# Kernel optimization log

Hardware: AMD Instinct MI355X
Metric: run time of the kernel (lower is better)

Reference implementation:

```python
import jax, jax.numpy as jnp
import numpy as np

E = 8       # num experts
T = 1024    # num tokens
H = 1024    # hidden dim
I = 1024    # intermediate dim (per gate/up half)


def setup_inputs() -> dict:
    key = jax.random.key(0)
    k1, k2, k3, k4 = jax.random.split(key, 4)
    return {
        "hidden_states": jax.random.normal(k1, (T, H), jnp.float32),
        "router_logits": jax.random.normal(k2, (T, E), jnp.float32),
        # W13 stored pre-transposed as in the module: [E, H, 2*I]
        "W13": jax.random.normal(k3, (E, H, 2 * I), jnp.float32) * 0.02,
        # W2 stored pre-transposed: [E, I, H]
        "W2": jax.random.normal(k4, (E, I, H), jnp.float32) * 0.02,
        "top_k": 2,
    }


def reference(hidden_states, router_logits, W13, W2, top_k):
    num_experts = router_logits.shape[-1]
    # --- routing: topk_softmax (softmax over all experts, then top-k) ---
    probs = jax.nn.softmax(router_logits, axis=-1)            # [T, E]
    w, idx = jax.lax.top_k(probs, top_k)                      # [T, K]
    # renormalize=True path of moe_gather
    w = w / jnp.sum(w, axis=-1, keepdims=True)
    # combine weights per expert: [T, E]
    combine = jnp.sum(jax.nn.one_hot(idx, num_experts, dtype=w.dtype) * w[..., None], axis=1)
    # --- grouped gate-up GEMM + silu_and_mul ---
    h13 = jnp.einsum('th,ehf->tef', hidden_states, W13)       # [T, E, 2I]
    gate, up = jnp.split(h13, 2, axis=-1)                     # each [T, E, I]
    act = jax.nn.silu(gate) * up                              # silu_and_mul
    # --- grouped down GEMM ---
    down = jnp.einsum('tei,eih->teh', act, W2)                # [T, E, H]
    # --- combine (moe_gather) ---
    return jnp.einsum('te,teh->th', combine, down)            # [T, H]
```

## Files before the change

### kernel.cpp

```cpp
#include <hip/hip_runtime.h>
#include <hip/hip_bf16.h>
#include <stdint.h>

#define NE    8
#define NTOK  1024
#define NH    1024
#define NI    1024
#define NPAIR 2048

typedef __attribute__((ext_vector_type(8))) short short8;
typedef __attribute__((ext_vector_type(4))) float f32x4;
typedef unsigned short u16;
typedef unsigned int   u32;

__device__ __forceinline__ u16 f2bf(float x) {
    union { float f; u32 u; } v; v.f = x;
    return (u16)((v.u + 0x7fffu + ((v.u >> 16) & 1u)) >> 16);
}

__device__ __forceinline__ void async_ld16(u16* lds, const u16* g) {
    __builtin_amdgcn_global_load_lds(
        (const __attribute__((address_space(1))) u32*)g,
        (__attribute__((address_space(3))) u32*)lds, 16, 0, 0);
}

__global__ __launch_bounds__(256) void route_kernel(
    const float* __restrict__ logits,
    int* __restrict__ counts, int* __restrict__ pair_tok,
    int2* __restrict__ t2p, float2* __restrict__ t2w)
{
    __shared__ int s_cnt[NE];
    __shared__ int s_base[NE];
    const int tid = threadIdx.x;
    if (tid < NE) s_cnt[tid] = 0;
    __syncthreads();

    int eA[4][2]; int slotA[4][2]; float wA[4][2];

    #pragma unroll
    for (int i = 0; i < 4; i++) {
        const int t = tid * 4 + i;
        float l[NE];
        #pragma unroll
        for (int e = 0; e < NE; e++) l[e] = logits[t * NE + e];
        int i0 = 0;
        #pragma unroll
        for (int e = 1; e < NE; e++) if (l[e] > l[i0]) i0 = e;
        int i1 = -1;
        #pragma unroll
        for (int e = 0; e < NE; e++) {
            if (e == i0) continue;
            if (i1 < 0 || l[e] > l[i1]) i1 = e;
        }
        const float e10 = __expf(l[i1] - l[i0]);
        const float inv = 1.0f / (1.0f + e10);
        eA[i][0] = i0; eA[i][1] = i1;
        wA[i][0] = inv; wA[i][1] = e10 * inv;
        slotA[i][0] = atomicAdd(&s_cnt[i0], 1);
        slotA[i][1] = atomicAdd(&s_cnt[i1], 1);
    }
    __syncthreads();
    if (tid == 0) {
        int acc = 0;
        #pragma unroll
        for (int e = 0; e < NE; e++) { s_base[e] = acc; acc += s_cnt[e]; }
    }
    __syncthreads();
    if (tid < NE) counts[tid] = s_cnt[tid];
    #pragma unroll
    for (int i = 0; i < 4; i++) {
        const int t = tid * 4 + i;
        const int p0 = s_base[eA[i][0]] + slotA[i][0];
        const int p1 = s_base[eA[i][1]] + slotA[i][1];
        pair_tok[p0] = t;
        pair_tok[p1] = t;
        t2p[t] = make_int2(p0, p1);
        t2w[t] = make_float2(wA[i][0], wA[i][1]);
    }
}

__device__ __forceinline__ bool find_tile(
    const int* __restrict__ counts, int tile, int bm, int ntn,
    int& e_o, int& mt_o, int& nt_o, int& cnt_o, int& base_o)
{
    int base = 0;
    #pragma unroll
    for (int e = 0; e < NE; e++) {
        const int cnt = counts[e];
        const int mtiles = (cnt + bm - 1) / bm;
        const int tiles = mtiles * ntn;
        if (tile < tiles) {
            e_o = e; mt_o = tile / ntn; nt_o = tile - (tile / ntn) * ntn;
            cnt_o = cnt; base_o = base; return true;
        }
        tile -= tiles; base += cnt;
    }
    return false;
}

__global__ __launch_bounds__(256) void cvt_x_kernel(
    const float* __restrict__ src, u16* __restrict__ dst)
{
    const int i = blockIdx.x * 256 + threadIdx.x;
    const float4* s = (const float4*)src;
    const float4 a = s[2 * i], b = s[2 * i + 1];
    uint4 o;
    o.x = f2bf(a.x) | ((u32)f2bf(a.y) << 16);
    o.y = f2bf(a.z) | ((u32)f2bf(a.w) << 16);
    o.z = f2bf(b.x) | ((u32)f2bf(b.y) << 16);
    o.w = f2bf(b.z) | ((u32)f2bf(b.w) << 16);
    *(uint4*)(dst + (size_t)i * 8) = o;
}

__global__ __launch_bounds__(256) void cvt_tr_kernel(
    const float* __restrict__ src, u16* __restrict__ dst, int K, int N)
{
    __shared__ float Ts[64][65];
    const int ktiles = K >> 6, ntiles = N >> 6;
    const int tpe = ktiles * ntiles;
    const int e = blockIdx.x / tpe;
    const int rem = blockIdx.x - e * tpe;
    const int kt = rem / ntiles, nt = rem - (rem / ntiles) * ntiles;
    const float* sb = src + ((size_t)e * K + (size_t)kt * 64) * N + nt * 64;
    const int tid = threadIdx.x;

    #pragma unroll
    for (int i = 0; i < 4; i++) {
        const int idx = tid + i * 256;
        const int r = idx >> 4, c = (idx & 15) << 2;
        const float4 v = *(const float4*)(sb + (size_t)r * N + c);
        Ts[r][c + 0] = v.x; Ts[r][c + 1] = v.y;
        Ts[r][c + 2] = v.z; Ts[r][c + 3] = v.w;
    }
    __syncthreads();
    u16* db = dst + ((size_t)e * N + (size_t)nt * 64) * K + kt * 64;
    #pragma unroll
    for (int i = 0; i < 2; i++) {
        const int u = tid + i * 256;
        const int n = u >> 3, k8 = (u & 7) << 3;
        uint4 o;
        o.x = f2bf(Ts[k8 + 0][n]) | ((u32)f2bf(Ts[k8 + 1][n]) << 16);
        o.y = f2bf(Ts[k8 + 2][n]) | ((u32)f2bf(Ts[k8 + 3][n]) << 16);
        o.z = f2bf(Ts[k8 + 4][n]) | ((u32)f2bf(Ts[k8 + 5][n]) << 16);
        o.w = f2bf(Ts[k8 + 6][n]) | ((u32)f2bf(Ts[k8 + 7][n]) << 16);
        *(uint4*)(db + (size_t)n * K + k8) = o;
    }
}

__global__ __launch_bounds__(256) void gemm1_kernel(
    const u16* __restrict__ Xb, const u16* __restrict__ W13t,
    const int* __restrict__ counts, const int* __restrict__ pair_tok,
    u16* __restrict__ act)
{
    int e, mt, nt, cnt, base;
    if (!find_tile(counts, blockIdx.x, 128, NI / 64, e, mt, nt, cnt, base)) return;

    __shared__ u16 As[128 * 32];
    __shared__ u16 Bs[128 * 32];

    const int tid = threadIdx.x;
    const int ct = nt * 64;

    const int ra = tid >> 2, sa = (tid & 3) << 3;
    const int t0 = pair_tok[base + min(mt * 128 + ra, cnt - 1)];
    const int t1 = pair_tok[base + min(mt * 128 + 64 + ra, cnt - 1)];
    const u16* ga0 = Xb + (size_t)t0 * NH + sa;
    const u16* ga1 = Xb + (size_t)t1 * NH + sa;
    u16* la0 = As + tid * 8;
    u16* la1 = As + (tid + 256) * 8;

    const u16* gb0 = W13t + ((size_t)e * 2048 + ct + ra) * 1024 + sa;
    const u16* gb1 = W13t + ((size_t)e * 2048 + 1024 + ct + ra) * 1024 + sa;
    u16* lb0 = Bs + tid * 8;
    u16* lb1 = Bs + (tid + 256) * 8;

    const int lane = tid & 63, w = tid >> 6;
    const int quad = lane >> 4, lid = lane & 15;
    const int rw = w >> 1, cw = w & 1;

    const short8* afp[4];
    const short8* bgp[2];
    const short8* bup[2];
    #pragma unroll
    for (int mi = 0; mi < 4; mi++)
        afp[mi] = (const short8*)(As + (rw * 64 + mi * 16 + lid) * 32 + quad * 8);
    #pragma unroll
    for (int nj = 0; nj < 2; nj++) {
        bgp[nj] = (const short8*)(Bs + (cw * 32 + nj * 16 + lid) * 32 + quad * 8);
        bup[nj] = (const short8*)(Bs + (64 + cw * 32 + nj * 16 + lid) * 32 + quad * 8);
    }

    f32x4 accg[4][2] = {};
    f32x4 accu[4][2] = {};

    for (int k0 = 0; k0 < NH; k0 += 32) {
        async_ld16(la0, ga0 + k0);
        async_ld16(la1, ga1 + k0);
        async_ld16(lb0, gb0 + k0);
        async_ld16(lb1, gb1 + k0);
        __syncthreads();
        short8 a[4], bg[2], bu[2];
        #pragma unroll
        for (int mi = 0; mi < 4; mi++) a[mi] = *afp[mi];
        #pragma unroll
        for (int nj = 0; nj < 2; nj++) { bg[nj] = *bgp[nj]; bu[nj] = *bup[nj]; }
        #pragma unroll
        for (int mi = 0; mi < 4; mi++) {
            #pragma unroll
            for (int nj = 0; nj < 2; nj++) {
                accg[mi][nj] = __builtin_amdgcn_mfma_f32_16x16x32_bf16(a[mi], bg[nj], accg[mi][nj], 0, 0, 0);
                accu[mi][nj] = __builtin_amdgcn_mfma_f32_16x16x32_bf16(a[mi], bu[nj], accu[mi][nj], 0, 0, 0);
            }
        }
        __syncthreads();
    }

    #pragma unroll
    for (int mi = 0; mi < 4; mi++) {
        #pragma unroll
        for (int nj = 0; nj < 2; nj++) {
            const int col = ct + cw * 32 + nj * 16 + lid;
            #pragma unroll
            for (int r = 0; r < 4; r++) {
                const int row = mt * 128 + rw * 64 + mi * 16 + quad * 4 + r;
                if (row < cnt) {
                    const float g = accg[mi][nj][r], u = accu[mi][nj][r];
                    const float s = g / (1.0f + __expf(-g)) * u;
                    act[(size_t)(base + row) * NI + col] = f2bf(s);
                }
            }
        }
    }
}

__global__ __launch_bounds__(256) void gemm2_kernel(
    const u16* __restrict__ act, const u16* __restrict__ W2t,
    const int* __restrict__ counts, float* __restrict__ down)
{
    int e, mt, nt, cnt, base;
    if (!find_tile(counts, blockIdx.x, 64, NH / 128, e, mt, nt, cnt, base)) return;

    __shared__ u16 As[64 * 32];
    __shared__ u16 Bs[128 * 32];

    const int tid = threadIdx.x;
    const int ct = nt * 128;

    const int ra = tid >> 2, sa = (tid & 3) << 3;
    const int prow = base + min(mt * 64 + ra, cnt - 1);
    const u16* ga = act + (size_t)prow * NI + sa;
    u16* la = As + tid * 8;

    const u16* gb0 = W2t + ((size_t)e * 1024 + ct + ra) * NI + sa;
    const u16* gb1 = W2t + ((size_t)e * 1024 + ct + 64 + ra) * NI + sa;
    u16* lb0 = Bs + tid * 8;
    u16* lb1 = Bs + (tid + 256) * 8;

    const int lane = tid & 63, w = tid >> 6;
    const int quad = lane >> 4, lid = lane & 15;

    const short8* afp[4];
    const short8* bfp[2];
    #pragma unroll
    for (int mi = 0; mi < 4; mi++)
        afp[mi] = (const short8*)(As + (mi * 16 + lid) * 32 + quad * 8);
    #pragma unroll
    for (int nj = 0; nj < 2; nj++)
        bfp[nj] = (const short8*)(Bs + (w * 32 + nj * 16 + lid) * 32 + quad * 8);

    f32x4 acc[4][2] = {};

    for (int k0 = 0; k0 < NI; k0 += 32) {
        async_ld16(la, ga + k0);
        async_ld16(lb0, gb0 + k0);
        async_ld16(lb1, gb1 + k0);
        __syncthreads();
        short8 a[4], b[2];
        #pragma unroll
        for (int mi = 0; mi < 4; mi++) a[mi] = *afp[mi];
        #pragma unroll
        for (int nj = 0; nj < 2; nj++) b[nj] = *bfp[nj];
        #pragma unroll
        for (int mi = 0; mi < 4; mi++) {
            #pragma unroll
            for (int nj = 0; nj < 2; nj++)
                acc[mi][nj] = __builtin_amdgcn_mfma_f32_16x16x32_bf16(a[mi], b[nj], acc[mi][nj], 0, 0, 0);
        }
        __syncthreads();
    }

    #pragma unroll
    for (int mi = 0; mi < 4; mi++) {
        #pragma unroll
        for (int nj = 0; nj < 2; nj++) {
            const int col = ct + w * 32 + nj * 16 + lid;
            #pragma unroll
            for (int r = 0; r < 4; r++) {
                const int row = mt * 64 + mi * 16 + quad * 4 + r;
                if (row < cnt)
                    down[(size_t)(base + row) * NH + col] = acc[mi][nj][r];
            }
        }
    }
}

__global__ __launch_bounds__(256) void combine_kernel(
    const float* __restrict__ down, const int2* __restrict__ t2p,
    const float2* __restrict__ t2w, float* __restrict__ out)
{
    const int i = blockIdx.x * 256 + threadIdx.x;
    const int t = i >> 8;
    const int c = (i & 255) << 2;
    const int2 p = t2p[t];
    const float2 wv = t2w[t];
    const float4 d0 = *(const float4*)(down + (size_t)p.x * NH + c);
    const float4 d1 = *(const float4*)(down + (size_t)p.y * NH + c);
    float4 o;
    o.x = wv.x * d0.x + wv.y * d1.x;
    o.y = wv.x * d0.y + wv.y * d1.y;
    o.z = wv.x * d0.z + wv.y * d1.z;
    o.w = wv.x * d0.w + wv.y * d1.w;
    *(float4*)(out + (size_t)t * NH + c) = o;
}

extern "C" void kernel_launch(void* const* d_in, const int* in_sizes, int n_in,
                              void* d_out, int out_size, void* d_ws, size_t ws_size,
                              hipStream_t stream)
{
    const float* X      = (const float*)d_in[0];
    const float* logits = (const float*)d_in[1];
    const float* W13    = (const float*)d_in[2];
    const float* W2     = (const float*)d_in[3];
    float* out = (float*)d_out;

    char* ws = (char*)d_ws;
    int*    counts   = (int*)(ws + 0);
    int*    pair_tok = (int*)(ws + 256);
    int2*   t2p      = (int2*)(ws + 256 + 8192);
    float2* t2w      = (float2*)(ws + 256 + 16384);
    u16*    Xb       = (u16*)(ws + 65536);
    u16*    W13t     = (u16*)(ws + 4194304);
    u16*    W2t      = (u16*)(ws + 4194304 + 33554432);
    u16*    act      = (u16*)(ws + 54525952);
    float*  down     = (float*)(ws + 58720256);

    route_kernel<<<1, 256, 0, stream>>>(logits, counts, pair_tok, t2p, t2w);
    cvt_x_kernel<<<512, 256, 0, stream>>>(X, Xb);
    cvt_tr_kernel<<<NE * 16 * 32, 256, 0, stream>>>(W13, W13t, NH, 2 * NI);
    cvt_tr_kernel<<<NE * 16 * 16, 256, 0, stream>>>(W2, W2t, NI, NH);

    const int grid1 = (NPAIR / 128 + NE - 1) * (NI / 64);
    const int grid2 = (NPAIR / 64 + NE - 1) * (NH / 128);
    gemm1_kernel<<<grid1, 256, 0, stream>>>(Xb, W13t, counts, pair_tok, act);
    gemm2_kernel<<<grid2, 256, 0, stream>>>(act, W2t, counts, down);
    combine_kernel<<<NTOK * NH / 1024, 256, 0, stream>>>(down, t2p, t2w, out);
}
```

Before: 196.0 us.

## Fuse weight bf16 conversion into GEMMs and combine into gemm2 via atomics

Removes the separate transpose-and-convert kernels for W13 and W2. The GEMMs now read fp32 weights directly, convert them to bf16 in registers and store them into padded LDS, with a register prefetch of the next k-slice. This drops the extra full pass over the weights and the workspace writes. The combine kernel is also removed: gemm2 scales its results by the routing weight and atomically adds them into a zeroed output, which avoids the down buffer round trip but adds atomics and a memset. The fp32 weight loads are strided column reads, 4 bytes per lane, which may coalesce worse than the previous 16-byte async loads, and each weight is reloaded once per m-tile.

After: 205.1 us. 4.6% more time.

```diff
diff --git a/kernel.cpp b/kernel.cpp
--- a/kernel.cpp
+++ b/kernel.cpp
@@ -6,7 +6,9 @@
 #define NTOK  1024
 #define NH    1024
 #define NI    1024
+#define N13   2048
 #define NPAIR 2048
+#define SROW  40
 
 typedef __attribute__((ext_vector_type(8))) short short8;
 typedef __attribute__((ext_vector_type(4))) float f32x4;
@@ -18,16 +20,19 @@
     return (u16)((v.u + 0x7fffu + ((v.u >> 16) & 1u)) >> 16);
 }
 
-__device__ __forceinline__ void async_ld16(u16* lds, const u16* g) {
-    __builtin_amdgcn_global_load_lds(
-        (const __attribute__((address_space(1))) u32*)g,
-        (__attribute__((address_space(3))) u32*)lds, 16, 0, 0);
+__device__ __forceinline__ uint4 pack8(const float* f) {
+    uint4 o;
+    o.x = f2bf(f[0]) | ((u32)f2bf(f[1]) << 16);
+    o.y = f2bf(f[2]) | ((u32)f2bf(f[3]) << 16);
+    o.z = f2bf(f[4]) | ((u32)f2bf(f[5]) << 16);
+    o.w = f2bf(f[6]) | ((u32)f2bf(f[7]) << 16);
+    return o;
 }
 
 __global__ __launch_bounds__(256) void route_kernel(
     const float* __restrict__ logits,
     int* __restrict__ counts, int* __restrict__ pair_tok,
-    int2* __restrict__ t2p, float2* __restrict__ t2w)
+    float* __restrict__ pair_w)
 {
     __shared__ int s_cnt[NE];
     __shared__ int s_base[NE];
@@ -70,12 +75,12 @@
     #pragma unroll
     for (int i = 0; i < 4; i++) {
         const int t = tid * 4 + i;
-        const int p0 = s_base[eA[i][0]] + slotA[i][0];
-        const int p1 = s_base[eA[i][1]] + slotA[i][1];
-        pair_tok[p0] = t;
-        pair_tok[p1] = t;
-        t2p[t] = make_int2(p0, p1);
-        t2w[t] = make_float2(wA[i][0], wA[i][1]);
+        #pragma unroll
+        for (int k = 0; k < 2; k++) {
+            const int p = s_base[eA[i][k]] + slotA[i][k];
+            pair_tok[p] = t;
+            pair_w[p]   = wA[i][k];
+        }
     }
 }
 
@@ -104,106 +109,83 @@
     const int i = blockIdx.x * 256 + threadIdx.x;
     const float4* s = (const float4*)src;
     const float4 a = s[2 * i], b = s[2 * i + 1];
-    uint4 o;
-    o.x = f2bf(a.x) | ((u32)f2bf(a.y) << 16);
-    o.y = f2bf(a.z) | ((u32)f2bf(a.w) << 16);
-    o.z = f2bf(b.x) | ((u32)f2bf(b.y) << 16);
-    o.w = f2bf(b.z) | ((u32)f2bf(b.w) << 16);
-    *(uint4*)(dst + (size_t)i * 8) = o;
-}
-
-__global__ __launch_bounds__(256) void cvt_tr_kernel(
-    const float* __restrict__ src, u16* __restrict__ dst, int K, int N)
-{
-    __shared__ float Ts[64][65];
-    const int ktiles = K >> 6, ntiles = N >> 6;
-    const int tpe = ktiles * ntiles;
-    const int e = blockIdx.x / tpe;
-    const int rem = blockIdx.x - e * tpe;
-    const int kt = rem / ntiles, nt = rem - (rem / ntiles) * ntiles;
-    const float* sb = src + ((size_t)e * K + (size_t)kt * 64) * N + nt * 64;
-    const int tid = threadIdx.x;
-
-    #pragma unroll
-    for (int i = 0; i < 4; i++) {
-        const int idx = tid + i * 256;
-        const int r = idx >> 4, c = (idx & 15) << 2;
-        const float4 v = *(const float4*)(sb + (size_t)r * N + c);
-        Ts[r][c + 0] = v.x; Ts[r][c + 1] = v.y;
-        Ts[r][c + 2] = v.z; Ts[r][c + 3] = v.w;
-    }
-    __syncthreads();
-    u16* db = dst + ((size_t)e * N + (size_t)nt * 64) * K + kt * 64;
-    #pragma unroll
-    for (int i = 0; i < 2; i++) {
-        const int u = tid + i * 256;
-        const int n = u >> 3, k8 = (u & 7) << 3;
-        uint4 o;
-        o.x = f2bf(Ts[k8 + 0][n]) | ((u32)f2bf(Ts[k8 + 1][n]) << 16);
-        o.y = f2bf(Ts[k8 + 2][n]) | ((u32)f2bf(Ts[k8 + 3][n]) << 16);
-        o.z = f2bf(Ts[k8 + 4][n]) | ((u32)f2bf(Ts[k8 + 5][n]) << 16);
-        o.w = f2bf(Ts[k8 + 6][n]) | ((u32)f2bf(Ts[k8 + 7][n]) << 16);
-        *(uint4*)(db + (size_t)n * K + k8) = o;
-    }
+    float f[8] = {a.x, a.y, a.z, a.w, b.x, b.y, b.z, b.w};
+    *(uint4*)(dst + (size_t)i * 8) = pack8(f);
 }
 
 __global__ __launch_bounds__(256) void gemm1_kernel(
-    const u16* __restrict__ Xb, const u16* __restrict__ W13t,
+    const u16* __restrict__ Xb, const float* __restrict__ W13,
     const int* __restrict__ counts, const int* __restrict__ pair_tok,
     u16* __restrict__ act)
 {
     int e, mt, nt, cnt, base;
     if (!find_tile(counts, blockIdx.x, 128, NI / 64, e, mt, nt, cnt, base)) return;
 
-    __shared__ u16 As[128 * 32];
-    __shared__ u16 Bs[128 * 32];
+    __shared__ u16 As[128 * SROW];
+    __shared__ u16 Bs[128 * SROW];
 
     const int tid = threadIdx.x;
-    const int ct = nt * 64;
-
-    const int ra = tid >> 2, sa = (tid & 3) << 3;
-    const int t0 = pair_tok[base + min(mt * 128 + ra, cnt - 1)];
-    const int t1 = pair_tok[base + min(mt * 128 + 64 + ra, cnt - 1)];
-    const u16* ga0 = Xb + (size_t)t0 * NH + sa;
-    const u16* ga1 = Xb + (size_t)t1 * NH + sa;
-    u16* la0 = As + tid * 8;
-    u16* la1 = As + (tid + 256) * 8;
-
-    const u16* gb0 = W13t + ((size_t)e * 2048 + ct + ra) * 1024 + sa;
-    const u16* gb1 = W13t + ((size_t)e * 2048 + 1024 + ct + ra) * 1024 + sa;
-    u16* lb0 = Bs + tid * 8;
-    u16* lb1 = Bs + (tid + 256) * 8;
+    const int ct  = nt * 64;
+
+    const int ar = tid >> 2, aq = tid & 3;
+    const int t0 = pair_tok[base + min(mt * 128 + ar, cnt - 1)];
+    const int t1 = pair_tok[base + min(mt * 128 + 64 + ar, cnt - 1)];
+    const u16* ga0 = Xb + (size_t)t0 * NH + aq * 8;
+    const u16* ga1 = Xb + (size_t)t1 * NH + aq * 8;
+    u16* la0 = As + ar * SROW + aq * 8;
+    u16* la1 = As + (64 + ar) * SROW + aq * 8;
+
+    const int bn = tid & 127;
+    const int kh = tid >> 7;
+    const int gcol = (bn < 64) ? (ct + bn) : (NI + ct + bn - 64);
+    const float* gb = W13 + (size_t)e * NH * N13 + (size_t)kh * 16 * N13 + gcol;
+    u16* lb = Bs + bn * SROW + kh * 16;
 
     const int lane = tid & 63, w = tid >> 6;
     const int quad = lane >> 4, lid = lane & 15;
     const int rw = w >> 1, cw = w & 1;
 
-    const short8* afp[4];
-    const short8* bgp[2];
-    const short8* bup[2];
+    const u16* afp[4]; const u16* bgp[2]; const u16* bup[2];
     #pragma unroll
     for (int mi = 0; mi < 4; mi++)
-        afp[mi] = (const short8*)(As + (rw * 64 + mi * 16 + lid) * 32 + quad * 8);
+        afp[mi] = As + (rw * 64 + mi * 16 + lid) * SROW + quad * 8;
     #pragma unroll
     for (int nj = 0; nj < 2; nj++) {
-        bgp[nj] = (const short8*)(Bs + (cw * 32 + nj * 16 + lid) * 32 + quad * 8);
-        bup[nj] = (const short8*)(Bs + (64 + cw * 32 + nj * 16 + lid) * 32 + quad * 8);
+        bgp[nj] = Bs + (cw * 32 + nj * 16 + lid) * SROW + quad * 8;
+        bup[nj] = Bs + (64 + cw * 32 + nj * 16 + lid) * SROW + quad * 8;
     }
 
     f32x4 accg[4][2] = {};
     f32x4 accu[4][2] = {};
 
+    uint4 a0 = *(const uint4*)ga0;
+    uint4 a1 = *(const uint4*)ga1;
+    float bf[16];
+    #pragma unroll
+    for (int j = 0; j < 16; j++) bf[j] = gb[(size_t)j * N13];
+
     for (int k0 = 0; k0 < NH; k0 += 32) {
-        async_ld16(la0, ga0 + k0);
-        async_ld16(la1, ga1 + k0);
-        async_ld16(lb0, gb0 + k0);
-        async_ld16(lb1, gb1 + k0);
+        *(uint4*)la0 = a0;
+        *(uint4*)la1 = a1;
+        *(uint4*)lb       = pack8(bf);
+        *(uint4*)(lb + 8) = pack8(bf + 8);
         __syncthreads();
+
+        if (k0 + 32 < NH) {
+            a0 = *(const uint4*)(ga0 + k0 + 32);
+            a1 = *(const uint4*)(ga1 + k0 + 32);
+            #pragma unroll
+            for (int j = 0; j < 16; j++) bf[j] = gb[(size_t)(k0 + 32 + j) * N13];
+        }
+
         short8 a[4], bg[2], bu[2];
         #pragma unroll
-        for (int mi = 0; mi < 4; mi++) a[mi] = *afp[mi];
-        #pragma unroll
-        for (int nj = 0; nj < 2; nj++) { bg[nj] = *bgp[nj]; bu[nj] = *bup[nj]; }
+        for (int mi = 0; mi < 4; mi++) a[mi] = *(const short8*)afp[mi];
+        #pragma unroll
+        for (int nj = 0; nj < 2; nj++) {
+            bg[nj] = *(const short8*)bgp[nj];
+            bu[nj] = *(const short8*)bup[nj];
+        }
         #pragma unroll
         for (int mi = 0; mi < 4; mi++) {
             #pragma unroll
@@ -234,52 +216,64 @@
 }
 
 __global__ __launch_bounds__(256) void gemm2_kernel(
-    const u16* __restrict__ act, const u16* __restrict__ W2t,
-    const int* __restrict__ counts, float* __restrict__ down)
+    const u16* __restrict__ act, const float* __restrict__ W2,
+    const int* __restrict__ counts, const int* __restrict__ pair_tok,
+    const float* __restrict__ pair_w, float* __restrict__ out)
 {
     int e, mt, nt, cnt, base;
     if (!find_tile(counts, blockIdx.x, 64, NH / 128, e, mt, nt, cnt, base)) return;
 
-    __shared__ u16 As[64 * 32];
-    __shared__ u16 Bs[128 * 32];
+    __shared__ u16 As[64 * SROW];
+    __shared__ u16 Bs[128 * SROW];
 
     const int tid = threadIdx.x;
-    const int ct = nt * 128;
-
-    const int ra = tid >> 2, sa = (tid & 3) << 3;
-    const int prow = base + min(mt * 64 + ra, cnt - 1);
-    const u16* ga = act + (size_t)prow * NI + sa;
-    u16* la = As + tid * 8;
-
-    const u16* gb0 = W2t + ((size_t)e * 1024 + ct + ra) * NI + sa;
-    const u16* gb1 = W2t + ((size_t)e * 1024 + ct + 64 + ra) * NI + sa;
-    u16* lb0 = Bs + tid * 8;
-    u16* lb1 = Bs + (tid + 256) * 8;
+    const int ct  = nt * 128;
+
+    const int ar = tid >> 2, aq = tid & 3;
+    const int prow = base + min(mt * 64 + ar, cnt - 1);
+    const u16* ga = act + (size_t)prow * NI + aq * 8;
+    u16* la = As + ar * SROW + aq * 8;
+
+    const int bn = tid & 127;
+    const int kh = tid >> 7;
+    const float* gb = W2 + (size_t)e * NI * NH + (size_t)kh * 16 * NH + ct + bn;
+    u16* lb = Bs + bn * SROW + kh * 16;
 
     const int lane = tid & 63, w = tid >> 6;
     const int quad = lane >> 4, lid = lane & 15;
 
-    const short8* afp[4];
-    const short8* bfp[2];
+    const u16* afp[4]; const u16* bfp[2];
     #pragma unroll
     for (int mi = 0; mi < 4; mi++)
-        afp[mi] = (const short8*)(As + (mi * 16 + lid) * 32 + quad * 8);
+        afp[mi] = As + (mi * 16 + lid) * SROW + quad * 8;
     #pragma unroll
     for (int nj = 0; nj < 2; nj++)
-        bfp[nj] = (const short8*)(Bs + (w * 32 + nj * 16 + lid) * 32 + quad * 8);
+        bfp[nj] = Bs + (w * 32 + nj * 16 + lid) * SROW + quad * 8;
 
     f32x4 acc[4][2] = {};
 
+    uint4 a0 = *(const uint4*)ga;
+    float bf[16];
+    #pragma unroll
+    for (int j = 0; j < 16; j++) bf[j] = gb[(size_t)j * NH];
+
     for (int k0 = 0; k0 < NI; k0 += 32) {
-        async_ld16(la, ga + k0);
-        async_ld16(lb0, gb0 + k0);
-        async_ld16(lb1, gb1 + k0);
+        *(uint4*)la       = a0;
+        *(uint4*)lb       = pack8(bf);
+        *(uint4*)(lb + 8) = pack8(bf + 8);
         __syncthreads();
+
+        if (k0 + 32 < NI) {
+            a0 = *(const uint4*)(ga + k0 + 32);
+            #pragma unroll
+            for (int j = 0; j < 16; j++) bf[j] = gb[(size_t)(k0 + 32 + j) * NH];
+        }
+
         short8 a[4], b[2];
         #pragma unroll
-        for (int mi = 0; mi < 4; mi++) a[mi] = *afp[mi];
-        #pragma unroll
-        for (int nj = 0; nj < 2; nj++) b[nj] = *bfp[nj];
+        for (int mi = 0; mi < 4; mi++) a[mi] = *(const short8*)afp[mi];
+        #pragma unroll
+        for (int nj = 0; nj < 2; nj++) b[nj] = *(const short8*)bfp[nj];
         #pragma unroll
         for (int mi = 0; mi < 4; mi++) {
             #pragma unroll
@@ -292,35 +286,20 @@
     #pragma unroll
     for (int mi = 0; mi < 4; mi++) {
         #pragma unroll
-        for (int nj = 0; nj < 2; nj++) {
-            const int col = ct + w * 32 + nj * 16 + lid;
-            #pragma unroll
-            for (int r = 0; r < 4; r++) {
-                const int row = mt * 64 + mi * 16 + quad * 4 + r;
-                if (row < cnt)
-                    down[(size_t)(base + row) * NH + col] = acc[mi][nj][r];
+        for (int r = 0; r < 4; r++) {
+            const int row = mt * 64 + mi * 16 + quad * 4 + r;
+            if (row < cnt) {
+                const int p = base + row;
+                const int t = pair_tok[p];
+                const float wgt = pair_w[p];
+                #pragma unroll
+                for (int nj = 0; nj < 2; nj++) {
+                    const int col = ct + w * 32 + nj * 16 + lid;
+                    atomicAdd(out + (size_t)t * NH + col, wgt * acc[mi][nj][r]);
+                }
             }
         }
     }
-}
-
-__global__ __launch_bounds__(256) void combine_kernel(
-    const float* __restrict__ down, const int2* __restrict__ t2p,
-    const float2* __restrict__ t2w, float* __restrict__ out)
-{
-    const int i = blockIdx.x * 256 + threadIdx.x;
-    const int t = i >> 8;
-    const int c = (i & 255) << 2;
-    const int2 p = t2p[t];
-    const float2 wv = t2w[t];
-    const float4 d0 = *(const float4*)(down + (size_t)p.x * NH + c);
-    const float4 d1 = *(const float4*)(down + (size_t)p.y * NH + c);
-    float4 o;
-    o.x = wv.x * d0.x + wv.y * d1.x;
-    o.y = wv.x * d0.y + wv.y * d1.y;
-    o.z = wv.x * d0.z + wv.y * d1.z;
-    o.w = wv.x * d0.w + wv.y * d1.w;
-    *(float4*)(out + (size_t)t * NH + c) = o;
 }
 
 extern "C" void kernel_launch(void* const* d_in, const int* in_sizes, int n_in,
@@ -334,24 +313,18 @@
     float* out = (float*)d_out;
 
     char* ws = (char*)d_ws;
-    int*    counts   = (int*)(ws + 0);
-    int*    pair_tok = (int*)(ws + 256);
-    int2*   t2p      = (int2*)(ws + 256 + 8192);
-    float2* t2w      = (float2*)(ws + 256 + 16384);
-    u16*    Xb       = (u16*)(ws + 65536);
-    u16*    W13t     = (u16*)(ws + 4194304);
-    u16*    W2t      = (u16*)(ws + 4194304 + 33554432);
-    u16*    act      = (u16*)(ws + 54525952);
-    float*  down     = (float*)(ws + 58720256);
-
-    route_kernel<<<1, 256, 0, stream>>>(logits, counts, pair_tok, t2p, t2w);
+    int*   counts   = (int*)(ws + 0);
+    int*   pair_tok = (int*)(ws + 256);
+    float* pair_w   = (float*)(ws + 256 + 8192);
+    u16*   Xb       = (u16*)(ws + 65536);
+    u16*   act      = (u16*)(ws + 65536 + 2097152);
+
+    hipMemsetAsync(d_out, 0, (size_t)NTOK * NH * sizeof(float), stream);
+    route_kernel<<<1, 256, 0, stream>>>(logits, counts, pair_tok, pair_w);
     cvt_x_kernel<<<512, 256, 0, stream>>>(X, Xb);
-    cvt_tr_kernel<<<NE * 16 * 32, 256, 0, stream>>>(W13, W13t, NH, 2 * NI);
-    cvt_tr_kernel<<<NE * 16 * 16, 256, 0, stream>>>(W2, W2t, NI, NH);
 
     const int grid1 = (NPAIR / 128 + NE - 1) * (NI / 64);
     const int grid2 = (NPAIR / 64 + NE - 1) * (NH / 128);
-    gemm1_kernel<<<grid1, 256, 0, stream>>>(Xb, W13t, counts, pair_tok, act);
-    gemm2_kernel<<<grid2, 256, 0, stream>>>(act, W2t, counts, down);
-    combine_kernel<<<NTOK * NH / 1024, 256, 0, stream>>>(down, t2p, t2w, out);
-}
+    gemm1_kernel<<<grid1, 256, 0, stream>>>(Xb, W13, counts, pair_tok, act);
+    gemm2_kernel<<<grid2, 256, 0, stream>>>(act, W2, counts, pair_tok, pair_w, out);
+}
```
